# Kernel optimization log

Hardware: AMD Instinct MI355X
Metric: run time of the kernel (lower is better)

The kernel has to match this reference:

```python
import jax, jax.numpy as jnp
import numpy as np

N, IN_CH, OUT_CH, E = 100000, 256, 8, 6400000

def setup_inputs() -> dict:
    key = jax.random.key(0)
    k1, k2, k3, k4 = jax.random.split(key, 4)
    X = jax.random.normal(k1, (N, IN_CH), dtype=jnp.float32)
    edge_index = jax.random.randint(k2, (2, E), 0, N, dtype=jnp.int64)
    # torch Linear weights: [out_channels, in_channels], no bias
    W1 = jax.random.normal(k3, (OUT_CH, IN_CH), dtype=jnp.float32) / np.sqrt(IN_CH)
    W2 = jax.random.normal(k4, (OUT_CH, IN_CH), dtype=jnp.float32) / np.sqrt(IN_CH)
    return {"X": X, "edge_index": edge_index, "W1": W1, "W2": W2}

def reference(X, edge_index, W1, W2):
    # Project first ([N, out] is tiny), then gather -- same math as
    # W1(X[e0]) + W2(X[e1]) but avoids two [E, in_channels] intermediates.
    P1 = X @ W1.T  # [N, out]
    P2 = X @ W2.T  # [N, out]
    return P1[edge_index[0]] + P2[edge_index[1]]  # [E, out]
```

## Files before the change

### kernel.cpp

```cpp
#include <hip/hip_runtime.h>
#include <hip/hip_fp16.h>

#define IN_CH 256
#define OUT_CH 8
#define LROW 264

typedef float f32x4  __attribute__((ext_vector_type(4)));
typedef short short8v __attribute__((ext_vector_type(8)));
typedef short short4v __attribute__((ext_vector_type(4)));

__device__ __forceinline__ short f2bf(float f) {
    unsigned u = __float_as_uint(f);
    u += 0x7FFFu + ((u >> 16) & 1u);
    return (short)(u >> 16);
}

__global__ __launch_bounds__(256) void proj_kernel(
    const float* __restrict__ X,
    const float* __restrict__ W1,
    const float* __restrict__ W2,
    __half* __restrict__ P1h,
    __half* __restrict__ P2h,
    int n, int ntiles, int nwaves)
{
    __shared__ short Xs[4][16][LROW];

    const int wv   = threadIdx.x >> 6;
    const int lane = threadIdx.x & 63;
    const int gw   = (blockIdx.x * 256 + threadIdx.x) >> 6;

    const int o  = lane & 15;
    const int lk = lane >> 4;

    const float* wrow = (o < 8) ? (W1 + (size_t)o * IN_CH)
                                : (W2 + (size_t)(o - 8) * IN_CH);
    short8v bfr[8];
    #pragma unroll
    for (int kb = 0; kb < 8; ++kb) {
        float4 u = *(const float4*)(wrow + kb * 32 + lk * 8);
        float4 v = *(const float4*)(wrow + kb * 32 + lk * 8 + 4);
        short8v b;
        b[0] = f2bf(u.x); b[1] = f2bf(u.y); b[2] = f2bf(u.z); b[3] = f2bf(u.w);
        b[4] = f2bf(v.x); b[5] = f2bf(v.y); b[6] = f2bf(v.z); b[7] = f2bf(v.w);
        bfr[kb] = b;
    }

    for (int t = gw; t < ntiles; t += nwaves) {
        const int r0 = t * 16;

        #pragma unroll
        for (int i = 0; i < 16; ++i) {
            float4 x = make_float4(0.f, 0.f, 0.f, 0.f);
            if (r0 + i < n)
                x = *(const float4*)(X + (size_t)(r0 + i) * IN_CH + lane * 4);
            short4v s;
            s[0] = f2bf(x.x); s[1] = f2bf(x.y); s[2] = f2bf(x.z); s[3] = f2bf(x.w);
            *(short4v*)&Xs[wv][i][lane * 4] = s;
        }

        f32x4 acc = {0.f, 0.f, 0.f, 0.f};
        #pragma unroll
        for (int kb = 0; kb < 8; ++kb) {
            short8v a = *(const short8v*)&Xs[wv][o][kb * 32 + lk * 8];
            acc = __builtin_amdgcn_mfma_f32_16x16x32_bf16(a, bfr[kb], acc, 0, 0, 0);
        }

        #pragma unroll
        for (int r = 0; r < 4; ++r) {
            const int row = r0 + lk * 4 + r;
            if (row < n) {
                __half h = __float2half(acc[r]);
                if (o < 8) P1h[(size_t)row * OUT_CH + o] = h;
                else       P2h[(size_t)row * OUT_CH + (o - 8)] = h;
            }
        }
    }
}

__global__ __launch_bounds__(256) void gather_kernel(
    const int* __restrict__ e0,
    const int* __restrict__ e1,
    const uint4* __restrict__ T1,
    const uint4* __restrict__ T2,
    f32x4* __restrict__ outv,
    int E, int n)
{
    const int stride = gridDim.x * 256;
    const unsigned nmax = (unsigned)(n - 1);
    for (int e = blockIdx.x * 256 + threadIdx.x; e < E; e += stride) {
        unsigned i0 = (unsigned)__builtin_nontemporal_load(e0 + e);
        unsigned i1 = (unsigned)__builtin_nontemporal_load(e1 + e);
        i0 = i0 > nmax ? nmax : i0;
        i1 = i1 > nmax ? nmax : i1;

        uint4 a = T1[i0];
        uint4 b = T2[i1];
        const __half2* ah = (const __half2*)&a;
        const __half2* bh = (const __half2*)&b;

        float2 s0 = __half22float2(ah[0]);
        float2 s1 = __half22float2(ah[1]);
        float2 s2 = __half22float2(ah[2]);
        float2 s3 = __half22float2(ah[3]);
        float2 t0 = __half22float2(bh[0]);
        float2 t1 = __half22float2(bh[1]);
        float2 t2 = __half22float2(bh[2]);
        float2 t3 = __half22float2(bh[3]);

        f32x4 r0 = { s0.x + t0.x, s0.y + t0.y, s1.x + t1.x, s1.y + t1.y };
        f32x4 r1 = { s2.x + t2.x, s2.y + t2.y, s3.x + t3.x, s3.y + t3.y };

        size_t oi = 2u * (size_t)e;
        __builtin_nontemporal_store(r0, outv + oi);
        __builtin_nontemporal_store(r1, outv + oi + 1);
    }
}

extern "C" void kernel_launch(void* const* d_in, const int* in_sizes, int n_in,
                              void* d_out, int out_size, void* d_ws, size_t ws_size,
                              hipStream_t stream) {
    const float* X    = (const float*)d_in[0];
    const int*   eidx = (const int*)d_in[1];
    const float* W1   = (const float*)d_in[2];
    const float* W2   = (const float*)d_in[3];

    const int n = in_sizes[0] / IN_CH;
    const int E = in_sizes[1] / 2;

    __half* P1h = (__half*)d_ws;
    __half* P2h = P1h + (size_t)n * OUT_CH;

    const int ntiles = (n + 15) / 16;
    const int proj_blocks = 768;
    const int nwaves = proj_blocks * 4;
    proj_kernel<<<proj_blocks, 256, 0, stream>>>(
        X, W1, W2, P1h, P2h, n, ntiles, nwaves);

    const int gather_blocks = (E + 255) / 256;
    gather_kernel<<<gather_blocks, 256, 0, stream>>>(
        eidx, eidx + E, (const uint4*)P1h, (const uint4*)P2h,
        (f32x4*)d_out, E, n);
}
```

Before: 122.9 us.

## Split each edge across two lanes and exchange halves via shuffle in gather

The gather kernel now uses two threads per edge. Each lane loads one index and one projected row (from T1 or T2), swaps half of the row with its neighbour lane through a cross-lane shuffle, and writes one 16-byte output vector. Each wave then issues contiguous 16-byte stores and has twice as many independent gathers in flight. The cost is twice the thread count, extra shuffle instructions, and index loads whose per-instruction pattern now interleaves two distant arrays.

```diff
diff --git a/kernel.cpp b/kernel.cpp
--- a/kernel.cpp
+++ b/kernel.cpp
@@ -78,42 +78,39 @@
 }
 
 __global__ __launch_bounds__(256) void gather_kernel(
-    const int* __restrict__ e0,
-    const int* __restrict__ e1,
+    const int* __restrict__ eidx,
     const uint4* __restrict__ T1,
     const uint4* __restrict__ T2,
     f32x4* __restrict__ outv,
     int E, int n)
 {
-    const int stride = gridDim.x * 256;
+    const int t = blockIdx.x * 256 + threadIdx.x;
+    if (t >= 2 * E) return;
+
+    const int e     = t >> 1;
+    const int which = t & 1;
     const unsigned nmax = (unsigned)(n - 1);
-    for (int e = blockIdx.x * 256 + threadIdx.x; e < E; e += stride) {
-        unsigned i0 = (unsigned)__builtin_nontemporal_load(e0 + e);
-        unsigned i1 = (unsigned)__builtin_nontemporal_load(e1 + e);
-        i0 = i0 > nmax ? nmax : i0;
-        i1 = i1 > nmax ? nmax : i1;
 
-        uint4 a = T1[i0];
-        uint4 b = T2[i1];
-        const __half2* ah = (const __half2*)&a;
-        const __half2* bh = (const __half2*)&b;
+    const int* ip = eidx + (which ? E : 0);
+    unsigned idx = (unsigned)__builtin_nontemporal_load(ip + e);
+    idx = idx > nmax ? nmax : idx;
 
-        float2 s0 = __half22float2(ah[0]);
-        float2 s1 = __half22float2(ah[1]);
-        float2 s2 = __half22float2(ah[2]);
-        float2 s3 = __half22float2(ah[3]);
-        float2 t0 = __half22float2(bh[0]);
-        float2 t1 = __half22float2(bh[1]);
-        float2 t2 = __half22float2(bh[2]);
-        float2 t3 = __half22float2(bh[3]);
+    const uint4 row = which ? T2[idx] : T1[idx];
 
-        f32x4 r0 = { s0.x + t0.x, s0.y + t0.y, s1.x + t1.x, s1.y + t1.y };
-        f32x4 r1 = { s2.x + t2.x, s2.y + t2.y, s3.x + t3.x, s3.y + t3.y };
+    unsigned mine0 = which ? row.z : row.x;
+    unsigned mine1 = which ? row.w : row.y;
+    unsigned send0 = which ? row.x : row.z;
+    unsigned send1 = which ? row.y : row.w;
+    unsigned recv0 = (unsigned)__shfl_xor((int)send0, 1, 64);
+    unsigned recv1 = (unsigned)__shfl_xor((int)send1, 1, 64);
 
-        size_t oi = 2u * (size_t)e;
-        __builtin_nontemporal_store(r0, outv + oi);
-        __builtin_nontemporal_store(r1, outv + oi + 1);
-    }
+    float2 f0 = __half22float2(*(const __half2*)&mine0);
+    float2 f1 = __half22float2(*(const __half2*)&mine1);
+    float2 g0 = __half22float2(*(const __half2*)&recv0);
+    float2 g1 = __half22float2(*(const __half2*)&recv1);
+
+    f32x4 r = { f0.x + g0.x, f0.y + g0.y, f1.x + g1.x, f1.y + g1.y };
+    __builtin_nontemporal_store(r, outv + t);
 }
 
 extern "C" void kernel_launch(void* const* d_in, const int* in_sizes, int n_in,
@@ -136,8 +133,8 @@
     proj_kernel<<<proj_blocks, 256, 0, stream>>>(
         X, W1, W2, P1h, P2h, n, ntiles, nwaves);
 
-    const int gather_blocks = (E + 255) / 256;
+    const int gather_blocks = (2 * E + 255) / 256;
     gather_kernel<<<gather_blocks, 256, 0, stream>>>(
-        eidx, eidx + E, (const uint4*)P1h, (const uint4*)P2h,
+        eidx, (const uint4*)P1h, (const uint4*)P2h,
         (f32x4*)d_out, E, n);
 }
```

Result: slower. 136.3 us (+10.9%).
